# Optimization experiments

Hardware: AMD Instinct MI355X
Metric: run time of the kernel (lower is better)

The kernel has to match this reference:

```python
import jax, jax.numpy as jnp
import numpy as np

B, L, C, P, H, DK, MRD = 16, 1024, 512, 64, 8, 64, 7
STD = 0.02


def _layernorm(x, g, b):
    mu = x.mean(-1, keepdims=True)
    var = ((x - mu) ** 2).mean(-1, keepdims=True)
    return (x - mu) / jnp.sqrt(var + 1e-5) * g + b


def _rel_pos_table(L, m):
    i = jnp.arange(L)
    d = jnp.abs(i[:, None] - i[None, :]).astype(jnp.float32)
    d = jnp.where(d > m, m + jnp.log2(jnp.maximum(d - m, 1.0)), d)
    return jnp.clip(d, 0, 2 * m).astype(jnp.int32)  # (L, L) in [0, 2m]


def setup_inputs() -> dict:
    key = jax.random.key(0)
    ks = jax.random.split(key, 16)
    inp = {
        'qx': jax.random.normal(ks[0], (B, L, C), jnp.float32),
        'kx': jax.random.normal(ks[1], (B, L, C), jnp.float32),
        'vx': jax.random.normal(ks[2], (B, L, C), jnp.float32),
        'maskPAD': jnp.ones((B, L, L), jnp.int32),
        'Wp': jax.random.normal(ks[3], (C, P)) * STD,
        'bp': jnp.zeros((P,)),
        'WQ': jax.random.normal(ks[4], (C, H * DK)) * STD,
        'bQ': jnp.zeros((H * DK,)),
        'WK': jax.random.normal(ks[5], (C, H * DK)) * STD,
        'bK': jnp.zeros((H * DK,)),
        'WV': jax.random.normal(ks[6], (C, H * DK)) * STD,
        'bV': jnp.zeros((H * DK,)),
        'WO': jax.random.normal(ks[7], (H * DK, C)) * STD,
        'bO': jnp.zeros((C,)),
        'embK': jax.random.normal(ks[8], (2 * MRD + 1, H)) * STD,
        'embB': jax.random.normal(ks[9], (2 * MRD + 1, H)) * STD,
        'ln1_g': jnp.ones((C,)), 'ln1_b': jnp.zeros((C,)),
        'ln2_g': jnp.ones((C,)), 'ln2_b': jnp.zeros((C,)),
        'W1': jax.random.normal(ks[10], (C, 4 * C)) * STD,
        'b1': jnp.zeros((4 * C,)),
        'W2': jax.random.normal(ks[11], (4 * C, C)) * STD,
        'b2': jnp.zeros((C,)),
    }
    return inp


def reference(qx, kx, vx, maskPAD, Wp, bp, WQ, bQ, WK, bK, WV, bV, WO, bO,
              embK, embB, ln1_g, ln1_b, ln2_g, ln2_b, W1, b1, W2, b2):
    B_, L_, C_ = qx.shape
    P_ = Wp.shape[1]
    H_ = embK.shape[1]
    DK_ = WV.shape[1] // H_
    m = (embK.shape[0] - 1) // 2

    # pseudo-token attention pooling
    pScore = vx @ Wp + bp                                   # (B, L, P)
    pad = (maskPAD[:, 0] == 0)                              # (B, L)
    pScore = jnp.where(pad[:, :, None], -2.0 ** 15, pScore)
    pAlpha = jax.nn.softmax(pScore, axis=1)                 # softmax over L
    kxp = jnp.einsum('blp,blc->bpc', pAlpha, kx)            # (B, P, C)
    vxp = jnp.einsum('blp,blc->bpc', pAlpha, vx)
    pA = jax.lax.stop_gradient(pAlpha)                      # .detach()

    # multi-head attention vs pseudo tokens
    q = (qx @ WQ + bQ).reshape(B_, L_, H_, DK_).transpose(0, 2, 1, 3)   # (B,H,L,dk)
    k = (kxp @ WK + bK).reshape(B_, P_, H_, DK_).transpose(0, 2, 1, 3)  # (B,H,P,dk)
    v = (vxp @ WV + bV).reshape(B_, P_, H_, DK_).transpose(0, 2, 1, 3)
    scores = jnp.einsum('bhld,bhpd->bhlp', q, k) / np.sqrt(DK_).astype(np.float32)

    # relative position multiplicative/additive bias, pooled through pA
    tab = _rel_pos_table(L_, m)                             # (L, L)
    Krel = embK[tab].transpose(2, 0, 1)                     # (H, L, L)
    brel = embB[tab].transpose(2, 0, 1)
    Kb = jnp.einsum('hlm,bmp->bhlp', Krel, pA)
    bb = jnp.einsum('hlm,bmp->bhlp', brel, pA)
    scores = scores * Kb + bb

    alpha = jax.nn.softmax(scores, axis=3)
    z = jnp.einsum('bhlp,bhpd->bhld', alpha, v)
    z = z.transpose(0, 2, 1, 3).reshape(B_, L_, H_ * DK_)
    z = z @ WO + bO

    # FFN block (residuals against vx, post-LN)
    z1 = _layernorm(vx + z, ln1_g, ln1_b)
    ffn = jax.nn.gelu(z1 @ W1 + b1, approximate=False) @ W2 + b2
    x = _layernorm(z1 + ffn, ln2_g, ln2_b)
    return x
```

## Files before the change

### kernel.cpp

```cpp
#include <hip/hip_runtime.h>
#include <hip/hip_bf16.h>

#define BI   16
#define LSEQ 1024
#define CDIM 512
#define PDIM 64
#define HH   8
#define DKK  64

typedef __hip_bfloat16 bf16;
typedef unsigned short u16;
typedef __attribute__((ext_vector_type(8))) short bf16x8;
typedef __attribute__((ext_vector_type(4))) float f32x4;

__constant__ int c_dlo[15] = {0,1,2,3,4,5,6,7, 9,11,15,23,39, 71,135};
__constant__ int c_dhi[15] = {0,1,2,3,4,5,6,8,10,14,22,38,70,134,1023};

__device__ __forceinline__ float b2f(u16 u) {
    union { unsigned int i; float f; } c; c.i = ((unsigned int)u) << 16; return c.f;
}
__device__ __forceinline__ u16 f2bu(float v) {
    bf16 h = __float2bfloat16(v);
    return *(u16*)&h;
}
__device__ __forceinline__ float ldDyn(const void* p, size_t i, int f) {
    return f ? ((const float*)p)[i] : b2f(((const u16*)p)[i]);
}
__device__ __forceinline__ void ld4Dyn(const void* p, size_t i, int f, float* o) {
    if (f) { float4 v = *(const float4*)((const float*)p + i);
             o[0]=v.x; o[1]=v.y; o[2]=v.z; o[3]=v.w; }
    else   { ushort4 u = *(const ushort4*)((const u16*)p + i);
             o[0]=b2f(u.x); o[1]=b2f(u.y); o[2]=b2f(u.z); o[3]=b2f(u.w); }
}

__device__ __forceinline__ void gll16(const u16* g, u16* l) {
    __builtin_amdgcn_global_load_lds(
        (const __attribute__((address_space(1))) unsigned int*)g,
        (__attribute__((address_space(3))) unsigned int*)l,
        16, 0, 0);
}

__device__ __forceinline__ float wsum(float v) {
    #pragma unroll
    for (int o = 32; o; o >>= 1) v += __shfl_xor(v, o, 64);
    return v;
}
__device__ __forceinline__ float wmax(float v) {
    #pragma unroll
    for (int o = 32; o; o >>= 1) v = fmaxf(v, __shfl_xor(v, o, 64));
    return v;
}

__device__ __forceinline__ float gelu_f(float v) {
    float x  = v * 0.70710678118654752f;
    float ax = fabsf(x);
    float t  = __builtin_amdgcn_rcpf(1.0f + 0.3275911f * ax);
    float p  = t * (0.254829592f + t * (-0.284496736f + t * (1.421413741f +
               t * (-1.453152027f + t * 1.061405429f))));
    float e  = __expf(-ax * ax);
    float er = 1.0f - p * e;
    er = (x < 0.0f) ? -er : er;
    return 0.5f * v * (1.0f + er);
}

__global__ void k_detect(const unsigned int* __restrict__ qw, int* __restrict__ flag) {
    __shared__ int cnt;
    if (threadIdx.x == 0) cnt = 0;
    __syncthreads();
    int local = 0;
    for (int i = threadIdx.x; i < 4096; i += 256) {
        float fv = b2f((u16)(qw[i] & 0xFFFFu));
        float af = fabsf(fv);
        if (fv == 0.0f || (af >= 0.0009765625f && af <= 32.0f)) local++;
    }
    atomicAdd(&cnt, local);
    __syncthreads();
    if (threadIdx.x == 0) flag[0] = (cnt >= 2048) ? 0 : 1;
}

__global__ __launch_bounds__(256) void k_cvt2(
    const void* __restrict__ s0, u16* __restrict__ d0,
    const void* __restrict__ s1, u16* __restrict__ d1,
    const int* __restrict__ flag, int n)
{
    const int fA = flag[0];
    const void* src = blockIdx.y ? s1 : s0;
    u16* dst = blockIdx.y ? d1 : d0;
    int i = (blockIdx.x * 256 + threadIdx.x) * 4;
    if (i >= n) return;
    float t[4]; ld4Dyn(src, i, fA, t);
    ushort4 o; o.x = f2bu(t[0]); o.y = f2bu(t[1]); o.z = f2bu(t[2]); o.w = f2bu(t[3]);
    *(ushort4*)(dst + i) = o;
}

__device__ __forceinline__ void transp_core(
    const void* W, u16* WT, int fd, int Kd, int Nd, int bx, int by)
{
    __shared__ u16 t[32][33];
    const int tx = threadIdx.x & 31, ty = threadIdx.x >> 5;
    #pragma unroll
    for (int r = 0; r < 32; r += 8) {
        int k = by * 32 + ty + r, n = bx * 32 + tx;
        t[ty + r][tx] = f2bu(ldDyn(W, (size_t)k * Nd + n, fd));
    }
    __syncthreads();
    #pragma unroll
    for (int r = 0; r < 32; r += 8) {
        int n = bx * 32 + ty + r, k = by * 32 + tx;
        WT[(size_t)n * Kd + k] = t[tx][ty + r];
    }
}

__global__ __launch_bounds__(256) void k_transp(
    const void* __restrict__ W, u16* __restrict__ WT, const int* __restrict__ flag,
    int Kd, int Nd)
{
    transp_core(W, WT, flag[0], Kd, Nd, blockIdx.x, blockIdx.y);
}

__global__ __launch_bounds__(256) void k_transp4(
    const void* __restrict__ W0, u16* __restrict__ T0,
    const void* __restrict__ W1, u16* __restrict__ T1,
    const void* __restrict__ W2, u16* __restrict__ T2,
    const void* __restrict__ W3, u16* __restrict__ T3,
    const int* __restrict__ flag)
{
    const void* W; u16* T;
    switch (blockIdx.z) {
        case 0: W = W0; T = T0; break;
        case 1: W = W1; T = T1; break;
        case 2: W = W2; T = T2; break;
        default: W = W3; T = T3; break;
    }
    transp_core(W, T, flag[0], 512, 512, blockIdx.x, blockIdx.y);
}

__global__ __launch_bounds__(256) void k_transpcv(
    const void* __restrict__ kx, const u16* __restrict__ vxb,
    u16* __restrict__ kxT, u16* __restrict__ vxT, const int* __restrict__ flag)
{
    const int t = blockIdx.z >> 4;
    const int b = blockIdx.z & 15;
    const int l0 = blockIdx.x * 64, c0 = blockIdx.y * 32;
    __shared__ u16 s[32][72];
    const int tid = threadIdx.x;
    if (t == 0) {
        const int fd = flag[0];
        #pragma unroll
        for (int p = 0; p < 2; ++p) {
            int l = (tid >> 3) + p * 32, c4 = (tid & 7) * 4;
            float v[4];
            ld4Dyn(kx, ((size_t)b * LSEQ + l0 + l) * CDIM + c0 + c4, fd, v);
            #pragma unroll
            for (int k = 0; k < 4; ++k) s[c4 + k][l] = f2bu(v[k]);
        }
    } else {
        #pragma unroll
        for (int p = 0; p < 2; ++p) {
            int l = (tid >> 3) + p * 32, c4 = (tid & 7) * 4;
            ushort4 u = *(const ushort4*)&vxb[((size_t)b * LSEQ + l0 + l) * CDIM + c0 + c4];
            s[c4 + 0][l] = u.x; s[c4 + 1][l] = u.y;
            s[c4 + 2][l] = u.z; s[c4 + 3][l] = u.w;
        }
    }
    __syncthreads();
    u16* dst = t ? vxT : kxT;
    #pragma unroll
    for (int p = 0; p < 2; ++p) {
        int c = (tid >> 4) + p * 16, l4 = (tid & 15) * 4;
        *(ushort4*)&dst[((size_t)b * CDIM + c0 + c) * LSEQ + l0 + l4] =
            *(const ushort4*)&s[c][l4];
    }
}

__device__ __forceinline__ void gemm_core(
    u16 (*As)[32], u16 (*Bs)[32],
    const u16* A, const u16* BT, const void* bias, const u16* res, void* Cc, int fd,
    int K, int lda, int ldbt, int ldc, size_t bOff, int mode, int outBf, int perm,
    int m0, int n0)
{
    const int tid = threadIdx.x;
    const int wave = tid >> 6, lane = tid & 63;
    const int q = lane >> 4, l16 = lane & 15;
    const int wm = (wave >> 2) * 64, wn = (wave & 3) * 64;
    const int srow = lane >> 2;
    const int scol = ((lane & 3) ^ ((lane >> 3) & 3)) * 8;
    const int rchk = (l16 >> 1) & 3;
    const int nt = K >> 5;

    f32x4 acc[4][4];
    #pragma unroll
    for (int i = 0; i < 4; ++i)
        #pragma unroll
        for (int j = 0; j < 4; ++j) acc[i][j] = (f32x4){0.f, 0.f, 0.f, 0.f};

    auto stage = [&](int t, int buf) {
        gll16(A + (size_t)(m0 + wave * 16 + srow) * lda + t * 32 + scol,
              &As[buf * 128 + wave * 16][0]);
        #pragma unroll
        for (int pass = 0; pass < 2; ++pass)
            gll16(BT + (size_t)(n0 + pass * 128 + wave * 16 + srow) * ldbt + t * 32 + scol,
                  &Bs[buf * 256 + pass * 128 + wave * 16][0]);
    };

    stage(0, 0);

    for (int t = 0; t < nt; ++t) {
        if (t + 1 < nt) {
            stage(t + 1, (t + 1) & 1);
            asm volatile("s_waitcnt vmcnt(3)" ::: "memory");
        } else {
            asm volatile("s_waitcnt vmcnt(0)" ::: "memory");
        }
        __builtin_amdgcn_sched_barrier(0);
        __builtin_amdgcn_s_barrier();

        const int ca = (t & 1) * 128, cbB = (t & 1) * 256;
        bf16x8 af[4], bfr[4];
        #pragma unroll
        for (int i = 0; i < 4; ++i)
            af[i] = *(const bf16x8*)&As[ca + wm + i * 16 + l16][(q ^ rchk) * 8];
        #pragma unroll
        for (int j = 0; j < 4; ++j)
            bfr[j] = *(const bf16x8*)&Bs[cbB + wn + j * 16 + l16][(q ^ rchk) * 8];
        #pragma unroll
        for (int i = 0; i < 4; ++i)
            #pragma unroll
            for (int j = 0; j < 4; ++j)
                acc[i][j] = __builtin_amdgcn_mfma_f32_16x16x32_bf16(af[i], bfr[j], acc[i][j], 0, 0, 0);

        if (t + 1 < nt) {
            asm volatile("s_waitcnt lgkmcnt(0)" ::: "memory");
            __builtin_amdgcn_sched_barrier(0);
            __builtin_amdgcn_s_barrier();
        }
    }

    float bv[4];
    #pragma unroll
    for (int j = 0; j < 4; ++j)
        bv[j] = ldDyn(bias, bOff + (size_t)(n0 + wn + j * 16 + l16), fd);

    #pragma unroll
    for (int i = 0; i < 4; ++i) {
        int row = m0 + wm + i * 16 + q * 4;
        #pragma unroll
        for (int j = 0; j < 4; ++j) {
            int col = n0 + wn + j * 16 + l16;
            #pragma unroll
            for (int r = 0; r < 4; ++r) {
                float v = acc[i][j][r] + bv[j];
                int m = row + r;
                if (mode == 2) {
                    v += b2f(res[(size_t)m * ldc + col]);
                    if (outBf) ((u16*)Cc)[(size_t)m * ldc + col] = f2bu(v);
                    else       ((float*)Cc)[(size_t)m * ldc + col] = v;
                } else {
                    if (mode == 1) v = gelu_f(v);
                    size_t idx = perm ? (size_t)((m >> 6) << 15) + ((size_t)col << 6) + (m & 63)
                                      : (size_t)m * ldc + col;
                    if (outBf) ((u16*)Cc)[idx] = f2bu(v);
                    else       ((float*)Cc)[idx] = v;
                }
            }
        }
    }
}

__global__ __launch_bounds__(512) void gemm_mfma(
    const u16* __restrict__ A, const u16* __restrict__ BT, const void* __restrict__ bias,
    const u16* __restrict__ res, void* __restrict__ Cc, const int* __restrict__ flag,
    int K, int lda, int ldbt, int ldc, size_t bOff, int mode, int outBf, int perm)
{
    __shared__ u16 As[256][32];
    __shared__ u16 Bs[512][32];
    const int lin = blockIdx.y * gridDim.x + blockIdx.x;
    const int chunk = (gridDim.x * gridDim.y) >> 3;
    const int wg = (lin & 7) * chunk + (lin >> 3);
    const int bx = wg % gridDim.x, by = wg / gridDim.x;
    gemm_core(As, Bs, A, BT, bias, res, Cc, flag[0], K, lda, ldbt, ldc, bOff,
              mode, outBf, perm, by * 128, bx * 256);
}

__global__ __launch_bounds__(512) void gemm_kv(
    const u16* __restrict__ A0, const u16* __restrict__ A1,
    const u16* __restrict__ BT0, const u16* __restrict__ BT1,
    const void* __restrict__ b0, const void* __restrict__ b1,
    void* __restrict__ C0, void* __restrict__ C1, const int* __restrict__ flag)
{
    __shared__ u16 As[256][32];
    __shared__ u16 Bs[512][32];
    const int z = blockIdx.z;
    gemm_core(As, Bs, z ? A1 : A0, z ? BT1 : BT0, z ? b1 : b0, nullptr,
              z ? C1 : C0, flag[0],
              CDIM, CDIM, CDIM, CDIM, 0, 0, 1, z ? 1 : 0,
              blockIdx.y * 128, blockIdx.x * 256);
}

__global__ __launch_bounds__(256) void gemm_pool(
    const u16* __restrict__ pAT, const u16* __restrict__ kxT,
    const u16* __restrict__ vxT, u16* __restrict__ kvxb)
{
    __shared__ u16 As[128][32];
    __shared__ u16 Bs[256][32];
    const int b = blockIdx.y;
    const int n0 = blockIdx.x * 128;
    const u16* Ag = pAT + (size_t)b * (PDIM * LSEQ);
    const u16* Bg = (blockIdx.z ? vxT : kxT) + (size_t)b * (CDIM * LSEQ);
    u16* Cg = kvxb + (size_t)blockIdx.z * 524288 + (size_t)b * (PDIM * CDIM);

    const int tid = threadIdx.x;
    const int wave = tid >> 6, lane = tid & 63;
    const int q = lane >> 4, l16 = lane & 15;
    const int wm = (wave >> 1) * 32, wn = (wave & 1) * 64;
    const int srow = lane >> 2, scol = (lane & 3) * 8;

    f32x4 acc[2][4];
    #pragma unroll
    for (int i = 0; i < 2; ++i)
        #pragma unroll
        for (int j = 0; j < 4; ++j) acc[i][j] = (f32x4){0.f, 0.f, 0.f, 0.f};

    gll16(Ag + (size_t)(wave * 16 + srow) * LSEQ + scol, &As[wave * 16][0]);
    #pragma unroll
    for (int pass = 0; pass < 2; ++pass)
        gll16(Bg + (size_t)(n0 + wave * 32 + pass * 16 + srow) * LSEQ + scol,
              &Bs[wave * 32 + pass * 16][0]);
    __syncthreads();

    int cur = 0;
    for (int k0 = 0; k0 < LSEQ; k0 += 32) {
        if (k0 + 32 < LSEQ) {
            const int na = (cur ^ 1) * 64, nb = (cur ^ 1) * 128;
            gll16(Ag + (size_t)(wave * 16 + srow) * LSEQ + (k0 + 32) + scol,
                  &As[na + wave * 16][0]);
            #pragma unroll
            for (int pass = 0; pass < 2; ++pass)
                gll16(Bg + (size_t)(n0 + wave * 32 + pass * 16 + srow) * LSEQ + (k0 + 32) + scol,
                      &Bs[nb + wave * 32 + pass * 16][0]);
        }
        const int ca = cur * 64, cb = cur * 128;
        bf16x8 af[2], bfr[4];
        #pragma unroll
        for (int i = 0; i < 2; ++i) af[i] = *(const bf16x8*)&As[ca + wm + i * 16 + l16][q * 8];
        #pragma unroll
        for (int j = 0; j < 4; ++j) bfr[j] = *(const bf16x8*)&Bs[cb + wn + j * 16 + l16][q * 8];
        #pragma unroll
        for (int i = 0; i < 2; ++i)
            #pragma unroll
            for (int j = 0; j < 4; ++j)
                acc[i][j] = __builtin_amdgcn_mfma_f32_16x16x32_bf16(af[i], bfr[j], acc[i][j], 0, 0, 0);
        __syncthreads();
        cur ^= 1;
    }

    #pragma unroll
    for (int i = 0; i < 2; ++i) {
        int row = wm + i * 16 + q * 4;
        #pragma unroll
        for (int j = 0; j < 4; ++j) {
            int col = n0 + wn + j * 16 + l16;
            #pragma unroll
            for (int r = 0; r < 4; ++r)
                Cg[(size_t)(row + r) * CDIM + col] = f2bu(acc[i][j][r]);
        }
    }
}

__global__ __launch_bounds__(256) void gemm_mfma64(
    const u16* __restrict__ A, const u16* __restrict__ BT, const void* __restrict__ bias,
    float* __restrict__ Cc, const int* __restrict__ flag,
    int K, int lda, int ldbt)
{
    const int fd = flag[0];
    __shared__ u16 As[256][32];
    __shared__ u16 Bs[128][32];
    const int m0 = blockIdx.y * 128;
    const int tid = threadIdx.x;
    const int wave = tid >> 6, lane = tid & 63;
    const int q = lane >> 4, l16 = lane & 15;
    const int wm = wave * 32;
    const int srow = wave * 16 + (lane >> 2);
    const int scol = (lane & 3) * 8;

    f32x4 acc[2][4];
    #pragma unroll
    for (int i = 0; i < 2; ++i)
        #pragma unroll
        for (int j = 0; j < 4; ++j) acc[i][j] = (f32x4){0.f, 0.f, 0.f, 0.f};

    #pragma unroll
    for (int pass = 0; pass < 2; ++pass) {
        int row = pass * 64 + srow;
        gll16(A + (size_t)(m0 + row) * lda + scol, &As[pass * 64 + wave * 16][0]);
    }
    gll16(BT + (size_t)srow * ldbt + scol, &Bs[wave * 16][0]);
    __syncthreads();

    int cur = 0;
    for (int k0 = 0; k0 < K; k0 += 32) {
        if (k0 + 32 < K) {
            const int na = (cur ^ 1) * 128, nb = (cur ^ 1) * 64;
            #pragma unroll
            for (int pass = 0; pass < 2; ++pass) {
                int row = pass * 64 + srow;
                gll16(A + (size_t)(m0 + row) * lda + (k0 + 32) + scol,
                      &As[na + pass * 64 + wave * 16][0]);
            }
            gll16(BT + (size_t)srow * ldbt + (k0 + 32) + scol, &Bs[nb + wave * 16][0]);
        }
        const int ca = cur * 128, cb = cur * 64;
        bf16x8 af[2], bfr[4];
        #pragma unroll
        for (int i = 0; i < 2; ++i) af[i] = *(const bf16x8*)&As[ca + wm + i * 16 + l16][q * 8];
        #pragma unroll
        for (int j = 0; j < 4; ++j) bfr[j] = *(const bf16x8*)&Bs[cb + j * 16 + l16][q * 8];
        #pragma unroll
        for (int i = 0; i < 2; ++i)
            #pragma unroll
            for (int j = 0; j < 4; ++j)
                acc[i][j] = __builtin_amdgcn_mfma_f32_16x16x32_bf16(af[i], bfr[j], acc[i][j], 0, 0, 0);
        __syncthreads();
        cur ^= 1;
    }

    #pragma unroll
    for (int i = 0; i < 2; ++i) {
        int row = m0 + wm + i * 16 + q * 4;
        #pragma unroll
        for (int j = 0; j < 4; ++j) {
            int col = j * 16 + l16;
            #pragma unroll
            for (int r = 0; r < 4; ++r)
                Cc[(size_t)(row + r) * 64 + col] = acc[i][j][r] + ldDyn(bias, col, fd);
        }
    }
}

__global__ __launch_bounds__(256) void gemm_att(
    const u16* __restrict__ Abase, const u16* __restrict__ Bbase,
    void* __restrict__ outp, int mode)
{
    __shared__ u16 Aq[2][128][32];
    __shared__ u16 Bk[2][64][32];
    const int bh = blockIdx.y;
    const int b = bh >> 3, h = bh & 7;
    const int m0 = blockIdx.x * 128;
    const int tid = threadIdx.x;
    const int wave = tid >> 6, lane = tid & 63;
    const int q = lane >> 4, l16 = lane & 15;

    const u16* Ag; const u16* Bg; int lda, ldb;
    if (mode == 0) {
        Ag = Abase + ((size_t)b * LSEQ + m0) * CDIM + h * 64;  lda = CDIM;
        Bg = Bbase + (size_t)b * 32768 + h * 64;               ldb = CDIM;
    } else {
        Ag = Abase + ((size_t)bh * LSEQ + m0) * 64;            lda = 64;
        Bg = Bbase + (size_t)b * 32768 + (size_t)h * 64 * 64;  ldb = 64;
    }

    const int srow = lane >> 2;
    const int scol = (lane & 3) * 8;
    #pragma unroll
    for (int half = 0; half < 2; ++half) {
        #pragma unroll
        for (int pass = 0; pass < 2; ++pass) {
            int row = pass * 64 + wave * 16 + srow;
            gll16(Ag + (size_t)row * lda + half * 32 + scol,
                  &Aq[half][pass * 64 + wave * 16][0]);
        }
        gll16(Bg + (size_t)(wave * 16 + srow) * ldb + half * 32 + scol,
              &Bk[half][wave * 16][0]);
    }
    __syncthreads();

    f32x4 acc[2][4];
    #pragma unroll
    for (int i = 0; i < 2; ++i)
        #pragma unroll
        for (int j = 0; j < 4; ++j) acc[i][j] = (f32x4){0.f, 0.f, 0.f, 0.f};

    #pragma unroll
    for (int kk = 0; kk < 2; ++kk) {
        bf16x8 af[2], bfr[4];
        #pragma unroll
        for (int i = 0; i < 2; ++i)
            af[i] = *(const bf16x8*)&Aq[kk][wave * 32 + i * 16 + l16][q * 8];
        #pragma unroll
        for (int j = 0; j < 4; ++j)
            bfr[j] = *(const bf16x8*)&Bk[kk][j * 16 + l16][q * 8];
        #pragma unroll
        for (int i = 0; i < 2; ++i)
            #pragma unroll
            for (int j = 0; j < 4; ++j)
                acc[i][j] = __builtin_amdgcn_mfma_f32_16x16x32_bf16(af[i], bfr[j], acc[i][j], 0, 0, 0);
    }

    #pragma unroll
    for (int i = 0; i < 2; ++i) {
        int row = m0 + wave * 32 + i * 16 + q * 4;
        #pragma unroll
        for (int j = 0; j < 4; ++j) {
            int col = j * 16 + l16;
            #pragma unroll
            for (int r = 0; r < 4; ++r) {
                if (mode == 0) {
                    ((float*)outp)[((size_t)bh * LSEQ + row + r) * 64 + col] =
                        0.125f * acc[i][j][r];
                } else {
                    ((u16*)outp)[((size_t)b * LSEQ + row + r) * CDIM + h * 64 + col] =
                        f2bu(acc[i][j][r]);
                }
            }
        }
    }
}

__global__ __launch_bounds__(256) void k_softscan(
    const float* __restrict__ psc, const int* __restrict__ maskPAD,
    u16* __restrict__ pAT, float* __restrict__ cumT)
{
    const int b = blockIdx.x >> 6;
    const int p = blockIdx.x & 63;
    const int tid = threadIdx.x;
    __shared__ float s0[1024], s1[1024];
    __shared__ float redA[4], redB[4];

    float acc[4];
    #pragma unroll
    for (int r = 0; r < 4; ++r) {
        int m = tid + r * 256;
        float a = psc[((size_t)b * LSEQ + m) * PDIM + p];
        if (maskPAD[(size_t)b * LSEQ * LSEQ + m] == 0) a = -32768.0f;
        acc[r] = a;
    }
    float mx = fmaxf(fmaxf(acc[0], acc[1]), fmaxf(acc[2], acc[3]));
    mx = wmax(mx);
    if ((tid & 63) == 0) redA[tid >> 6] = mx;
    __syncthreads();
    mx = fmaxf(fmaxf(redA[0], redA[1]), fmaxf(redA[2], redA[3]));

    float e[4], ls = 0.f;
    #pragma unroll
    for (int r = 0; r < 4; ++r) { e[r] = expf(acc[r] - mx); ls += e[r]; }
    ls = wsum(ls);
    if ((tid & 63) == 0) redB[tid >> 6] = ls;
    __syncthreads();
    float inv = 1.0f / (redB[0] + redB[1] + redB[2] + redB[3]);

    #pragma unroll
    for (int r = 0; r < 4; ++r) {
        int m = tid + r * 256;
        float pa = e[r] * inv;
        pAT[((size_t)b * PDIM + p) * LSEQ + m] = f2bu(pa);
        s0[m] = pa;
    }
    __syncthreads();

    float* src = s0; float* dst = s1;
    for (int off = 1; off < 1024; off <<= 1) {
        #pragma unroll
        for (int r = 0; r < 4; ++r) {
            int i = tid + r * 256;
            float v = src[i];
            if (i >= off) v += src[i - off];
            dst[i] = v;
        }
        __syncthreads();
        float* t = src; src = dst; dst = t;
    }
    size_t cb = (size_t)b * (LSEQ + 1) * PDIM + p;
    if (tid == 0) cumT[cb] = 0.f;
    #pragma unroll
    for (int r = 0; r < 4; ++r) {
        int i = tid + r * 256;
        cumT[cb + (size_t)(i + 1) * PDIM] = src[i];
    }
}

__global__ __launch_bounds__(512) void k_sm(
    const float* __restrict__ raw, u16* __restrict__ alb,
    const float* __restrict__ cumT,
    const void* __restrict__ embK, const void* __restrict__ embB,
    const int* __restrict__ flag)
{
    const int fd = flag[0];
    const int b = blockIdx.x >> 10;
    const int l = blockIdx.x & 1023;
    const int tid = threadIdx.x;
    __shared__ float S[15][PDIM];
    __shared__ float eK[120], eB[120];

    if (tid < 120) { eK[tid] = ldDyn(embK, tid, fd); eB[tid] = ldDyn(embB, tid, fd); }

    const float* cb = cumT + (size_t)b * (LSEQ + 1) * PDIM;
    for (int idx = tid; idx < 960; idx += 512) {
        int t = idx >> 6, pp = idx & 63;
        float s;
        if (t == 0) {
            s = cb[(size_t)(l + 1) * 64 + pp] - cb[(size_t)l * 64 + pp];
        } else {
            s = 0.f;
            int hi = l - c_dlo[t];
            int lo = l - c_dhi[t]; if (lo < 0) lo = 0;
            if (hi >= lo) s += cb[(size_t)(hi + 1) * 64 + pp] - cb[(size_t)lo * 64 + pp];
            lo = l + c_dlo[t];
            hi = l + c_dhi[t]; if (hi > 1023) hi = 1023;
            if (lo <= hi) s += cb[(size_t)(hi + 1) * 64 + pp] - cb[(size_t)lo * 64 + pp];
        }
        S[t][pp] = s;
    }
    __syncthreads();

    const int h = tid >> 6, p = tid & 63;
    float kbm = 0.f, bbm = 0.f;
    #pragma unroll
    for (int t = 0; t < 15; ++t) {
        float sv = S[t][p];
        kbm += eK[t * 8 + h] * sv;
        bbm += eB[t * 8 + h] * sv;
    }
    size_t idx = (((size_t)b * 8 + h) * LSEQ + l) * 64 + p;
    float sc = raw[idx] * kbm + bbm;
    float mx = wmax(sc);
    float e  = expf(sc - mx);
    float ssum = wsum(e);
    alb[idx] = f2bu(e / ssum);
}

__global__ __launch_bounds__(512) void k_ln4(
    const void* __restrict__ a, const u16* __restrict__ badd,
    const void* __restrict__ g, const void* __restrict__ be, const int* __restrict__ flag,
    void* __restrict__ out, int aKind, int outKind)
{
    const int fd = flag[0];
    const int fA = (aKind == 2) ? fd : aKind;
    const int fO = (outKind == 2) ? fd : outKind;
    const int tid = threadIdx.x;
    const int sub = tid >> 7;
    const int ln  = tid & 127;
    const size_t row  = (size_t)blockIdx.x * 4 + sub;
    const size_t base = row * CDIM + ln * 4;

    float x[4];
    ld4Dyn(a, base, fA, x);
    if (badd) {
        ushort4 u = *(const ushort4*)&badd[base];
        x[0] += b2f(u.x); x[1] += b2f(u.y); x[2] += b2f(u.z); x[3] += b2f(u.w);
    }

    __shared__ float r1[8], r2[8];
    const int wv = tid >> 6;
    float s = wsum(x[0] + x[1] + x[2] + x[3]);
    if ((tid & 63) == 0) r1[wv] = s;
    __syncthreads();
    float mu = (r1[sub * 2] + r1[sub * 2 + 1]) * (1.0f / 512.0f);

    float dv[4], s2 = 0.f;
    #pragma unroll
    for (int k = 0; k < 4; ++k) { dv[k] = x[k] - mu; s2 += dv[k] * dv[k]; }
    s2 = wsum(s2);
    if ((tid & 63) == 0) r2[wv] = s2;
    __syncthreads();
    float inv = rsqrtf((r2[sub * 2] + r2[sub * 2 + 1]) * (1.0f / 512.0f) + 1e-5f);

    float gg[4], bb[4];
    ld4Dyn(g,  (size_t)ln * 4, fd, gg);
    ld4Dyn(be, (size_t)ln * 4, fd, bb);

    float y[4];
    #pragma unroll
    for (int k = 0; k < 4; ++k) y[k] = dv[k] * inv * gg[k] + bb[k];

    if (fO) {
        float4 o; o.x = y[0]; o.y = y[1]; o.z = y[2]; o.w = y[3];
        *(float4*)((float*)out + base) = o;
    } else {
        ushort4 o; o.x = f2bu(y[0]); o.y = f2bu(y[1]); o.z = f2bu(y[2]); o.w = f2bu(y[3]);
        *(ushort4*)((u16*)out + base) = o;
    }
}

extern "C" void kernel_launch(void* const* d_in, const int* in_sizes, int n_in,
                              void* d_out, int out_size, void* d_ws, size_t ws_size,
                              hipStream_t stream)
{
    (void)in_sizes; (void)n_in; (void)out_size; (void)ws_size;
    const void* qx   = d_in[0];
    const void* kx   = d_in[1];
    const void* vx   = d_in[2];
    const int*  mask = (const int*)d_in[3];
    const void* Wp   = d_in[4];
    const void* bp   = d_in[5];
    const void* WQ   = d_in[6];
    const void* bQ   = d_in[7];
    const void* WK   = d_in[8];
    const void* bK   = d_in[9];
    const void* WV   = d_in[10];
    const void* bV   = d_in[11];
    const void* WO   = d_in[12];
    const void* bO   = d_in[13];
    const void* embK = d_in[14];
    const void* embB = d_in[15];
    const void* l1g  = d_in[16];
    const void* l1b  = d_in[17];
    const void* l2g  = d_in[18];
    const void* l2b  = d_in[19];
    const void* W1   = d_in[20];
    const void* b1   = d_in[21];
    const void* W2   = d_in[22];
    const void* b2   = d_in[23];

    float* ws     = (float*)d_ws;
    int*   flag   = (int*)d_ws;
    u16*   outFb  = (u16*)(ws + 64);
    float* psc    = ws + 64;
    float* cumT   = ws + 1048640;
    u16*   pAT    = (u16*)(ws + 2098240);
    u16*   kbh    = (u16*)(ws + 2622528);
    u16*   vbT    = (u16*)(ws + 2884672);
    u16*   albuf  = (u16*)(ws + 3146816);
    u16*   kvxb   = (u16*)(ws + 7341120);
    u16*   qz     = (u16*)(ws + 8388672);
    u16*   hidden = (u16*)(ws + 12582976);
    u16*   qxb    = hidden;
    u16*   zo     = qxb;
    u16*   vxb    = (u16*)(ws + 16777280);
    u16*   kxT    = (u16*)(ws + 20971584);
    u16*   vxT    = (u16*)(ws + 25165888);
    float* rawbuf = ws + 20971584;
    u16*   WqT    = (u16*)(ws + 29360192);
    u16*   WkT    = (u16*)(ws + 29491264);
    u16*   WvT    = (u16*)(ws + 29622336);
    u16*   WoT    = (u16*)(ws + 29753408);
    u16*   W1T    = (u16*)(ws + 29884480);
    u16*   W2T    = (u16*)(ws + 30408768);
    u16*   WpT    = (u16*)(ws + 30933056);

    const int MROW = BI * LSEQ;

    k_detect<<<dim3(1), dim3(256), 0, stream>>>((const unsigned int*)qx, flag);
    k_cvt2<<<dim3(MROW * CDIM / 1024, 2), dim3(256), 0, stream>>>(
        qx, qxb, vx, vxb, flag, MROW * CDIM);
    k_transp4<<<dim3(16, 16, 4), dim3(256), 0, stream>>>(
        WQ, WqT, WK, WkT, WV, WvT, WO, WoT, flag);
    k_transp<<<dim3(2, 16),  dim3(256), 0, stream>>>(Wp, WpT, flag, 512, 64);
    k_transp<<<dim3(64, 16), dim3(256), 0, stream>>>(W1, W1T, flag, 512, 2048);
    k_transp<<<dim3(16, 64), dim3(256), 0, stream>>>(W2, W2T, flag, 2048, 512);
    k_transpcv<<<dim3(16, 16, 32), dim3(256), 0, stream>>>(kx, vxb, kxT, vxT, flag);

    gemm_mfma64<<<dim3(1, MROW / 128), dim3(256), 0, stream>>>(
        vxb, WpT, bp, psc, flag, CDIM, CDIM, CDIM);
    k_softscan<<<dim3(BI * PDIM), dim3(256), 0, stream>>>(psc, mask, pAT, cumT);
    gemm_pool<<<dim3(4, 16, 2), dim3(256), 0, stream>>>(pAT, kxT, vxT, kvxb);
    gemm_mfma<<<dim3(2, MROW / 128), dim3(512), 0, stream>>>(
        qxb, WqT, bQ, nullptr, qz, flag, CDIM, CDIM, CDIM, CDIM, 0, 0, 1, 0);
    gemm_kv<<<dim3(2, 8, 2), dim3(512), 0, stream>>>(
        kvxb, kvxb + 524288, WkT, WvT, bK, bV, kbh, vbT, flag);
    gemm_att<<<dim3(8, BI * HH), dim3(256), 0, stream>>>(qz, kbh, rawbuf, 0);
    k_sm<<<dim3(BI * LSEQ), dim3(512), 0, stream>>>(
        rawbuf, albuf, cumT, embK, embB, flag);
    gemm_att<<<dim3(8, BI * HH), dim3(256), 0, stream>>>(albuf, vbT, qz, 1);
    gemm_mfma<<<dim3(2, MROW / 128), dim3(512), 0, stream>>>(
        qz, WoT, bO, nullptr, zo, flag, CDIM, CDIM, CDIM, CDIM, 0, 0, 1, 0);
    k_ln4<<<dim3(MROW / 4), dim3(512), 0, stream>>>(
        vx, zo, l1g, l1b, flag, qz, 2, 0);
    gemm_mfma<<<dim3(8, MROW / 128), dim3(512), 0, stream>>>(
        qz, W1T, b1, nullptr, hidden, flag, CDIM, CDIM, CDIM, 2048, 0, 1, 1, 0);
    gemm_mfma<<<dim3(2, MROW / 128), dim3(512), 0, stream>>>(
        hidden, W2T, b2, qz, outFb, flag, 2048, 2048, 2048, CDIM, 0, 2, 1, 0);
    k_ln4<<<dim3(MROW / 4), dim3(512), 0, stream>>>(
        outFb, nullptr, l2g, l2b, flag, d_out, 0, 2);
}
```

Before: 582.8 us.

## Triple-buffer GEMM LDS stages with prefetch distance two and split MFMA phases

Moves the shared MFMA GEMM core from double to triple buffering in LDS, so each tile is prefetched two K-steps ahead. The B-tile load for the future step is split across two points inside the iteration, interleaved with two halves of the MFMA work. The MFMA blocks run under raised wave priority via s_setprio. This is meant to hide global-load latency and drop the trailing barrier per K-step, at the cost of 1.5x more LDS per block, which may limit occupancy.

```diff
diff --git a/kernel.cpp b/kernel.cpp
--- a/kernel.cpp
+++ b/kernel.cpp
@@ -194,46 +194,63 @@
         #pragma unroll
         for (int j = 0; j < 4; ++j) acc[i][j] = (f32x4){0.f, 0.f, 0.f, 0.f};
 
-    auto stage = [&](int t, int buf) {
+    auto stageA = [&](int t, int buf) {
         gll16(A + (size_t)(m0 + wave * 16 + srow) * lda + t * 32 + scol,
               &As[buf * 128 + wave * 16][0]);
-        #pragma unroll
-        for (int pass = 0; pass < 2; ++pass)
-            gll16(BT + (size_t)(n0 + pass * 128 + wave * 16 + srow) * ldbt + t * 32 + scol,
-                  &Bs[buf * 256 + pass * 128 + wave * 16][0]);
     };
-
-    stage(0, 0);
+    auto stageB = [&](int t, int buf, int pass) {
+        gll16(BT + (size_t)(n0 + pass * 128 + wave * 16 + srow) * ldbt + t * 32 + scol,
+              &Bs[buf * 256 + pass * 128 + wave * 16][0]);
+    };
+
+    stageA(0, 0); stageB(0, 0, 0); stageB(0, 0, 1);
+    stageA(1, 1); stageB(1, 1, 0); stageB(1, 1, 1);
 
     for (int t = 0; t < nt; ++t) {
-        if (t + 1 < nt) {
-            stage(t + 1, (t + 1) & 1);
-            asm volatile("s_waitcnt vmcnt(3)" ::: "memory");
-        } else {
-            asm volatile("s_waitcnt vmcnt(0)" ::: "memory");
-        }
+        if (t + 1 < nt) asm volatile("s_waitcnt vmcnt(3)" ::: "memory");
+        else            asm volatile("s_waitcnt vmcnt(0)" ::: "memory");
         __builtin_amdgcn_sched_barrier(0);
         __builtin_amdgcn_s_barrier();
-
-        const int ca = (t & 1) * 128, cbB = (t & 1) * 256;
-        bf16x8 af[4], bfr[4];
-        #pragma unroll
-        for (int i = 0; i < 4; ++i)
-            af[i] = *(const bf16x8*)&As[ca + wm + i * 16 + l16][(q ^ rchk) * 8];
+        __builtin_amdgcn_sched_barrier(0);
+
+        const int nb = (t + 2) % 3;
+        if (t + 2 < nt) { stageA(t + 2, nb); stageB(t + 2, nb, 0); }
+
+        const int ca = (t % 3) * 128, cbB = (t % 3) * 256;
+        bf16x8 af0, af1, bfr[4];
+        af0 = *(const bf16x8*)&As[ca + wm + 0 * 16 + l16][(q ^ rchk) * 8];
+        af1 = *(const bf16x8*)&As[ca + wm + 1 * 16 + l16][(q ^ rchk) * 8];
         #pragma unroll
         for (int j = 0; j < 4; ++j)
             bfr[j] = *(const bf16x8*)&Bs[cbB + wn + j * 16 + l16][(q ^ rchk) * 8];
-        #pragma unroll
-        for (int i = 0; i < 4; ++i)
-            #pragma unroll
-            for (int j = 0; j < 4; ++j)
-                acc[i][j] = __builtin_amdgcn_mfma_f32_16x16x32_bf16(af[i], bfr[j], acc[i][j], 0, 0, 0);
-
-        if (t + 1 < nt) {
-            asm volatile("s_waitcnt lgkmcnt(0)" ::: "memory");
-            __builtin_amdgcn_sched_barrier(0);
-            __builtin_amdgcn_s_barrier();
-        }
+        asm volatile("s_waitcnt lgkmcnt(0)" ::: "memory");
+        __builtin_amdgcn_sched_barrier(0);
+        __builtin_amdgcn_s_setprio(1);
+        #pragma unroll
+        for (int j = 0; j < 4; ++j)
+            acc[0][j] = __builtin_amdgcn_mfma_f32_16x16x32_bf16(af0, bfr[j], acc[0][j], 0, 0, 0);
+        #pragma unroll
+        for (int j = 0; j < 4; ++j)
+            acc[1][j] = __builtin_amdgcn_mfma_f32_16x16x32_bf16(af1, bfr[j], acc[1][j], 0, 0, 0);
+        __builtin_amdgcn_s_setprio(0);
+        __builtin_amdgcn_s_barrier();
+        __builtin_amdgcn_sched_barrier(0);
+
+        if (t + 2 < nt) stageB(t + 2, nb, 1);
+
+        bf16x8 af2, af3;
+        af2 = *(const bf16x8*)&As[ca + wm + 2 * 16 + l16][(q ^ rchk) * 8];
+        af3 = *(const bf16x8*)&As[ca + wm + 3 * 16 + l16][(q ^ rchk) * 8];
+        asm volatile("s_waitcnt lgkmcnt(0)" ::: "memory");
+        __builtin_amdgcn_sched_barrier(0);
+        __builtin_amdgcn_s_setprio(1);
+        #pragma unroll
+        for (int j = 0; j < 4; ++j)
+            acc[2][j] = __builtin_amdgcn_mfma_f32_16x16x32_bf16(af2, bfr[j], acc[2][j], 0, 0, 0);
+        #pragma unroll
+        for (int j = 0; j < 4; ++j)
+            acc[3][j] = __builtin_amdgcn_mfma_f32_16x16x32_bf16(af3, bfr[j], acc[3][j], 0, 0, 0);
+        __builtin_amdgcn_s_setprio(0);
     }
 
     float bv[4];
@@ -272,8 +289,8 @@
     const u16* __restrict__ res, void* __restrict__ Cc, const int* __restrict__ flag,
     int K, int lda, int ldbt, int ldc, size_t bOff, int mode, int outBf, int perm)
 {
-    __shared__ u16 As[256][32];
-    __shared__ u16 Bs[512][32];
+    __shared__ u16 As[384][32];
+    __shared__ u16 Bs[768][32];
     const int lin = blockIdx.y * gridDim.x + blockIdx.x;
     const int chunk = (gridDim.x * gridDim.y) >> 3;
     const int wg = (lin & 7) * chunk + (lin >> 3);
@@ -288,8 +305,8 @@
     const void* __restrict__ b0, const void* __restrict__ b1,
     void* __restrict__ C0, void* __restrict__ C1, const int* __restrict__ flag)
 {
-    __shared__ u16 As[256][32];
-    __shared__ u16 Bs[512][32];
+    __shared__ u16 As[384][32];
+    __shared__ u16 Bs[768][32];
     const int z = blockIdx.z;
     gemm_core(As, Bs, z ? A1 : A0, z ? BT1 : BT0, z ? b1 : b0, nullptr,
               z ? C1 : C0, flag[0],
```

Result: slower. 606.9 us (+4.1%).
